# Optimization experiments

Hardware: AMD Instinct MI355X
Metric: run time of the kernel (lower is better)

## Reference

```python
import jax, jax.numpy as jnp
import numpy as np

B, N, K = 16, 2048, 20
NUM_PART = 16  # number of object classes for the one-hot label
NP = 50        # num_part (per-point part labels)
NEG_SLOPE = 0.2


def graph_feature(x, k):
    """DGCNN get_graph_feature. x: [B,C,N] -> [B,2C,N,k]."""
    xx = jnp.sum(x * x, axis=1)                      # [B,N]
    inner = jnp.einsum('bcn,bcm->bnm', x, x)         # [B,N,N]
    # negative squared distance (larger = closer)
    d = 2.0 * inner - xx[:, :, None] - xx[:, None, :]
    idx = jax.lax.top_k(d, k)[1]                     # [B,N,k] int32
    xt = jnp.transpose(x, (0, 2, 1))                 # [B,N,C]
    nbr = jax.vmap(lambda f, i: f[i])(xt, idx)       # [B,N,k,C] gather
    ctr = jnp.broadcast_to(xt[:, :, None, :], nbr.shape)
    feat = jnp.concatenate([nbr - ctr, ctr], axis=-1)  # [B,N,k,2C]
    return jnp.transpose(feat, (0, 3, 1, 2))         # [B,2C,N,k]


def cbr2d(x, w, s, b):  # 1x1 conv2d + folded-BN affine + leaky_relu
    y = jnp.einsum('oc,bcnk->bonk', w, x)
    return jax.nn.leaky_relu(y * s[None, :, None, None] + b[None, :, None, None], NEG_SLOPE)


def cbr1d(x, w, s, b):  # 1x1 conv1d + folded-BN affine + leaky_relu
    y = jnp.einsum('oc,bcn->bon', w, x)
    return jax.nn.leaky_relu(y * s[None, :, None] + b[None, :, None], NEG_SLOPE)


def setup_inputs() -> dict:
    key = jax.random.key(0)
    ks = jax.random.split(key, 40)
    ki = iter(range(40))

    def w(shape):
        fan_in = shape[1]
        return jax.random.normal(ks[next(ki)], shape, jnp.float32) * np.float32(np.sqrt(2.0 / fan_in))

    def sb(c):
        s = 1.0 + 0.1 * jax.random.normal(ks[next(ki)], (c,), jnp.float32)
        b = 0.1 * jax.random.normal(ks[next(ki)], (c,), jnp.float32)
        return s, b

    inp = {}
    inp['points'] = jax.random.normal(ks[next(ki)], (B, 3, N), jnp.float32)
    cls = jax.random.randint(ks[next(ki)], (B,), 0, NUM_PART)
    inp['cls_label'] = jax.nn.one_hot(cls, NUM_PART, dtype=jnp.float32)

    inp['w1'] = w((64, 6));    inp['s1'], inp['b1'] = sb(64)
    inp['w2'] = w((64, 64));   inp['s2'], inp['b2'] = sb(64)
    inp['w3'] = w((64, 128));  inp['s3'], inp['b3'] = sb(64)
    inp['w4'] = w((64, 64));   inp['s4'], inp['b4'] = sb(64)
    inp['w5'] = w((64, 128));  inp['s5'], inp['b5'] = sb(64)
    inp['w6'] = w((1024, 192)); inp['s6'], inp['b6'] = sb(1024)
    inp['wc'] = w((64, 16));   inp['sc'], inp['bc'] = sb(64)
    inp['wf1'] = w((256, 1024 + 64 + 192)); inp['sf1'], inp['bf1'] = sb(256)
    inp['wf2'] = w((256, 256)); inp['sf2'], inp['bf2'] = sb(256)
    inp['wf3'] = w((128, 256)); inp['sf3'], inp['bf3'] = sb(128)
    inp['wf4'] = w((NP, 128))
    return inp


def reference(points, cls_label,
              w1, s1, b1, w2, s2, b2, w3, s3, b3, w4, s4, b4, w5, s5, b5,
              w6, s6, b6, wc, sc, bc,
              wf1, sf1, bf1, wf2, sf2, bf2, wf3, sf3, bf3, wf4):
    # EdgeConv block 1
    x = graph_feature(points, K)                # [B,6,N,K]
    x = cbr2d(x, w1, s1, b1)
    x = cbr2d(x, w2, s2, b2)
    x1 = jnp.max(x, axis=-1)                    # [B,64,N]
    # EdgeConv block 2
    x = graph_feature(x1, K)                    # [B,128,N,K]
    x = cbr2d(x, w3, s3, b3)
    x = cbr2d(x, w4, s4, b4)
    x2 = jnp.max(x, axis=-1)
    # EdgeConv block 3
    x = graph_feature(x2, K)
    x = cbr2d(x, w5, s5, b5)
    x3 = jnp.max(x, axis=-1)

    xc = jnp.concatenate([x1, x2, x3], axis=1)  # [B,192,N]
    g = cbr1d(xc, w6, s6, b6)                   # [B,1024,N]
    g = jnp.max(g, axis=-1, keepdims=True)      # [B,1024,1]
    g = jnp.broadcast_to(g, (g.shape[0], 1024, N))

    oh = jnp.broadcast_to(cls_label[:, :, None], (cls_label.shape[0], 16, N))
    cv = cbr1d(oh, wc, sc, bc)                  # [B,64,N]

    x = jnp.concatenate([g, cv, x1, x2, x3], axis=1)  # [B,1280,N]
    feat = cbr1d(x, wf1, sf1, bf1)              # dropout = identity (eval)
    feat = cbr1d(feat, wf2, sf2, bf2)
    feat = cbr1d(feat, wf3, sf3, bf3)
    out = jnp.einsum('oc,bcn->bon', wf4, feat)  # [B,NP,N]
    out = jax.nn.log_softmax(out, axis=1)
    return jnp.transpose(out, (0, 2, 1))        # [B,N,NP]
```

## Files before the change

kernel.cpp:

```cpp
#include <hip/hip_runtime.h>

constexpr int PTS = 2048;
constexpr int KK  = 20;

typedef __attribute__((ext_vector_type(8))) short bf8;
typedef __attribute__((ext_vector_type(4))) float f32x4;

static __device__ __forceinline__ float lrelu(float x) { return fmaxf(x, 0.2f * x); }
static __device__ __forceinline__ float rl(float v, int l) {
  return __int_as_float(__builtin_amdgcn_readlane(__float_as_int(v), l));
}
static __device__ __forceinline__ unsigned cvt2(float lo, float hi) {
  unsigned r;
  asm("v_cvt_pk_bf16_f32 %0, %1, %2" : "=v"(r) : "v"(lo), "v"(hi));
  return r;
}
static __device__ __forceinline__ unsigned cvt2lo(float a, float b, unsigned h) {
  return cvt2(a - __uint_as_float(h << 16), b - __uint_as_float(h & 0xffff0000u));
}
static __device__ __forceinline__ unsigned short rne_bf16(float v) {
  unsigned u = __float_as_uint(v);
  return (unsigned short)((u + 0x7fffu + ((u >> 16) & 1u)) >> 16);
}
static __device__ __forceinline__ float bf2f(unsigned short u) {
  return __uint_as_float(((unsigned)u) << 16);
}
static __device__ __forceinline__ int swz(int row, int slot) {
  return slot ^ (row & 3) ^ ((row >> 2) & 3);
}
static __device__ __forceinline__ void argmax64(float& v, int& m) {
#pragma unroll
  for (int mask = 1; mask < 64; mask <<= 1) {
    float ov = __shfl_xor(v, mask, 64);
    int om = __shfl_xor(m, mask, 64);
    if (ov > v || (ov == v && om < m)) { v = ov; m = om; }
  }
}

template <int C>
__global__ __launch_bounds__(256) void xnorm_k(const float* __restrict__ x, float* __restrict__ xx) {
  const int i = blockIdx.x * 256 + threadIdx.x;
  const int b = i >> 11, m = i & 2047;
  float s = 0.f;
#pragma unroll
  for (int c = 0; c < C; ++c) {
    const float v = x[((long long)b * C + c) * PTS + m];
    s = fmaf(v, v, s);
  }
  xx[i] = s;
}

template <int C>
__global__ __launch_bounds__(256, 4) void fknn4_k(const float* __restrict__ x, const float* __restrict__ xx,
                                                  int* __restrict__ idxout) {
  __shared__ float dist[4][2112];
  __shared__ float xns[4][68];
  const int tid = threadIdx.x, lane = tid & 63, wid = tid >> 6;
  const int b = blockIdx.y;
  const int n0 = blockIdx.x * 4;

  if (tid < 4 * C) {
    const int p = tid & 3, c = tid >> 2;
    xns[p][c] = x[((long long)b * C + c) * PTS + n0 + p];
  }
  __syncthreads();

  float acc[4][2][4] = {};
  const float* px0 = x + (long long)b * C * PTS + (2 * wid) * 256 + 4 * lane;
  const float* px1 = px0 + 256;
#pragma unroll 4
  for (int c = 0; c < C; ++c) {
    const f32x4 v0 = *(const f32x4*)(px0 + (long long)c * PTS);
    const f32x4 v1 = *(const f32x4*)(px1 + (long long)c * PTS);
    const float xn0 = xns[0][c], xn1 = xns[1][c], xn2 = xns[2][c], xn3 = xns[3][c];
#pragma unroll
    for (int i = 0; i < 4; ++i) {
      acc[0][0][i] = fmaf(xn0, v0[i], acc[0][0][i]);
      acc[1][0][i] = fmaf(xn1, v0[i], acc[1][0][i]);
      acc[2][0][i] = fmaf(xn2, v0[i], acc[2][0][i]);
      acc[3][0][i] = fmaf(xn3, v0[i], acc[3][0][i]);
      acc[0][1][i] = fmaf(xn0, v1[i], acc[0][1][i]);
      acc[1][1][i] = fmaf(xn1, v1[i], acc[1][1][i]);
      acc[2][1][i] = fmaf(xn2, v1[i], acc[2][1][i]);
      acc[3][1][i] = fmaf(xn3, v1[i], acc[3][1][i]);
    }
  }
#pragma unroll
  for (int tt = 0; tt < 2; ++tt) {
    const f32x4 xv = *(const f32x4*)&xx[b * 2048 + (2 * wid + tt) * 256 + 4 * lane];
#pragma unroll
    for (int p = 0; p < 4; ++p)
#pragma unroll
      for (int i = 0; i < 4; ++i)
        dist[p][lane * 33 + 8 * wid + 4 * tt + i] = 2.f * acc[p][tt][i] - xv[i];
  }
  __syncthreads();

  const float NEG = -3.4e38f;
  float* dp = dist[wid];
  const int n = n0 + wid;
#define LDD(r) float d##r = dp[lane * 33 + r];
  LDD(0) LDD(1) LDD(2) LDD(3) LDD(4) LDD(5) LDD(6) LDD(7)
  LDD(8) LDD(9) LDD(10) LDD(11) LDD(12) LDD(13) LDD(14) LDD(15)
  LDD(16) LDD(17) LDD(18) LDD(19) LDD(20) LDD(21) LDD(22) LDD(23)
  LDD(24) LDD(25) LDD(26) LDD(27) LDD(28) LDD(29) LDD(30) LDD(31)
#undef LDD

#define P2(vA, iA, vB, iB, vO, iO) float vO = vA; int iO = iA; if (vB > vA) { vO = vB; iO = iB; }
#define TREE32(bvout, bsout)                                                            \
  {                                                                                     \
    P2(d0, 0, d1, 1, e0, j0) P2(d2, 2, d3, 3, e1, j1) P2(d4, 4, d5, 5, e2, j2)          \
    P2(d6, 6, d7, 7, e3, j3) P2(d8, 8, d9, 9, e4, j4) P2(d10, 10, d11, 11, e5, j5)      \
    P2(d12, 12, d13, 13, e6, j6) P2(d14, 14, d15, 15, e7, j7)                           \
    P2(d16, 16, d17, 17, e8, j8) P2(d18, 18, d19, 19, e9, j9)                           \
    P2(d20, 20, d21, 21, e10, j10) P2(d22, 22, d23, 23, e11, j11)                       \
    P2(d24, 24, d25, 25, e12, j12) P2(d26, 26, d27, 27, e13, j13)                       \
    P2(d28, 28, d29, 29, e14, j14) P2(d30, 30, d31, 31, e15, j15)                       \
    P2(e0, j0, e1, j1, f0, k0) P2(e2, j2, e3, j3, f1, k1)                               \
    P2(e4, j4, e5, j5, f2, k2) P2(e6, j6, e7, j7, f3, k3)                               \
    P2(e8, j8, e9, j9, f4, k4) P2(e10, j10, e11, j11, f5, k5)                           \
    P2(e12, j12, e13, j13, f6, k6) P2(e14, j14, e15, j15, f7, k7)                       \
    P2(f0, k0, f1, k1, g0, l0) P2(f2, k2, f3, k3, g1, l1)                               \
    P2(f4, k4, f5, k5, g2, l2) P2(f6, k6, f7, k7, g3, l3)                               \
    P2(g0, l0, g1, l1, h0, q0) P2(g2, l2, g3, l3, h1, q1)                               \
    P2(h0, q0, h1, q1, tf, ti)                                                          \
    bvout = tf;                                                                         \
    bsout = ti;                                                                         \
  }

  float c1v, c2v, c3v;
  int c1s, c2s, c3s;
  TREE32(c1v, c1s)
#define INVR(r) d##r = (c1s == r) ? NEG : d##r;
  INVR(0) INVR(1) INVR(2) INVR(3) INVR(4) INVR(5) INVR(6) INVR(7)
  INVR(8) INVR(9) INVR(10) INVR(11) INVR(12) INVR(13) INVR(14) INVR(15)
  INVR(16) INVR(17) INVR(18) INVR(19) INVR(20) INVR(21) INVR(22) INVR(23)
  INVR(24) INVR(25) INVR(26) INVR(27) INVR(28) INVR(29) INVR(30) INVR(31)
#undef INVR
  TREE32(c2v, c2s)
#define INVR(r) d##r = (c2s == r) ? NEG : d##r;
  INVR(0) INVR(1) INVR(2) INVR(3) INVR(4) INVR(5) INVR(6) INVR(7)
  INVR(8) INVR(9) INVR(10) INVR(11) INVR(12) INVR(13) INVR(14) INVR(15)
  INVR(16) INVR(17) INVR(18) INVR(19) INVR(20) INVR(21) INVR(22) INVR(23)
  INVR(24) INVR(25) INVR(26) INVR(27) INVR(28) INVR(29) INVR(30) INVR(31)
#undef INVR
  TREE32(c3v, c3s)
#define INVR(r) d##r = (c3s == r) ? NEG : d##r;
  INVR(0) INVR(1) INVR(2) INVR(3) INVR(4) INVR(5) INVR(6) INVR(7)
  INVR(8) INVR(9) INVR(10) INVR(11) INVR(12) INVR(13) INVR(14) INVR(15)
  INVR(16) INVR(17) INVR(18) INVR(19) INVR(20) INVR(21) INVR(22) INVR(23)
  INVR(24) INVR(25) INVR(26) INVR(27) INVR(28) INVR(29) INVR(30) INVR(31)
#undef INVR
  int c1m = ((c1s >> 2) << 8) + 4 * lane + (c1s & 3);
  int c2m = ((c2s >> 2) << 8) + 4 * lane + (c2s & 3);
  int c3m = ((c3s >> 2) << 8) + 4 * lane + (c3s & 3);

  int keep = 0;
  for (int rd = 0; rd < KK; ++rd) {
    float cv = c1v; int cm = c1m;
    argmax64(cv, cm);
    if (lane == rd) keep = cm;
    const int ol = (cm >> 2) & 63;
    const bool own = (lane == ol);
    if (own) { c1v = c2v; c1m = c2m; c2v = c3v; c2m = c3m; c3v = NEG; }
    const float oc1 = __shfl(c1v, ol, 64);
    if (oc1 == NEG) {
      float nv; int ns;
      TREE32(nv, ns)
      const int nm = ((ns >> 2) << 8) + 4 * lane + (ns & 3);
      if (own) { c1v = nv; c1m = nm; }
#define INVO(r) d##r = (own && ns == r) ? NEG : d##r;
      INVO(0) INVO(1) INVO(2) INVO(3) INVO(4) INVO(5) INVO(6) INVO(7)
      INVO(8) INVO(9) INVO(10) INVO(11) INVO(12) INVO(13) INVO(14) INVO(15)
      INVO(16) INVO(17) INVO(18) INVO(19) INVO(20) INVO(21) INVO(22) INVO(23)
      INVO(24) INVO(25) INVO(26) INVO(27) INVO(28) INVO(29) INVO(30) INVO(31)
#undef INVO
    }
  }
#undef TREE32
#undef P2
  if (lane < KK) idxout[((long long)b * PTS + n) * KK + lane] = keep;
}

__global__ __launch_bounds__(256) void prep_k(
    const float* __restrict__ w3, const float* __restrict__ s3, const float* __restrict__ b3,
    const float* __restrict__ w5, const float* __restrict__ s5, const float* __restrict__ b5,
    float* __restrict__ wc3, float* __restrict__ sc3, float* __restrict__ bc3,
    float* __restrict__ wc5, float* __restrict__ sc5, float* __restrict__ bc5) {
  const int i = blockIdx.x * 256 + threadIdx.x;
  const int half = i >> 13;
  const int r = i & 8191;
  const float* w = half ? w5 : w3;
  float* wcp = half ? wc5 : wc3;
  const int o = r >> 6, c = r & 63;
  wcp[r] = (o < 64) ? w[o * 128 + c] : (w[(o - 64) * 128 + 64 + c] - w[(o - 64) * 128 + c]);
  if (r < 128) {
    const float* s = half ? s5 : s3;
    const float* bb = half ? b5 : b3;
    float* scp = half ? sc5 : sc3;
    float* bcp = half ? bc5 : bc3;
    scp[r] = s[r & 63];
    bcp[r] = (r < 64) ? 0.f : bb[r - 64];
  }
}

__global__ __launch_bounds__(256) void wsplit_k(const float* __restrict__ w2, const float* __restrict__ w4,
                                                unsigned short* __restrict__ W2hi, unsigned short* __restrict__ W2lo,
                                                unsigned short* __restrict__ W4hi, unsigned short* __restrict__ W4lo) {
  const int i = blockIdx.x * 256 + threadIdx.x;
  const float v = (i < 4096) ? w2[i] : w4[i - 4096];
  const unsigned short h = rne_bf16(v);
  const unsigned short l = rne_bf16(v - bf2f(h));
  if (i < 4096) { W2hi[i] = h; W2lo[i] = l; }
  else { W4hi[i - 4096] = h; W4lo[i - 4096] = l; }
}

__global__ __launch_bounds__(256) void pq1_k(const float* __restrict__ pts,
    const float* __restrict__ w1, const float* __restrict__ s1, const float* __restrict__ b1,
    float* __restrict__ PQ) {
  const int i = blockIdx.x * 256 + threadIdx.x;
  const int o = i & 63;
  const int bn = i >> 6;
  const int b = bn >> 11, n = bn & 2047;
  const float* pb = pts + (long long)b * 3 * PTS;
  const float x = pb[n], y = pb[PTS + n], z = pb[2 * PTS + n];
  const float s = s1[o];
  const float wa0 = w1[o * 6], wa1 = w1[o * 6 + 1], wa2 = w1[o * 6 + 2];
  const float wb0 = w1[o * 6 + 3], wb1 = w1[o * 6 + 4], wb2 = w1[o * 6 + 5];
  PQ[(long long)bn * 128 + o] = s * (wa0 * x + wa1 * y + wa2 * z);
  PQ[(long long)bn * 128 + 64 + o] =
      fmaf(s, (wb0 - wa0) * x + (wb1 - wa1) * y + (wb2 - wa2) * z, b1[o]);
}

static __device__ __forceinline__ void mkfrag2(const float4 p0, const float4 p1,
                                               const float4 q0, const float4 q1,
                                               bf8& hi, bf8& lo) {
  const float y[8] = {p0.x + q0.x, p0.y + q0.y, p0.z + q0.z, p0.w + q0.w,
                      p1.x + q1.x, p1.y + q1.y, p1.z + q1.z, p1.w + q1.w};
  union { unsigned u[4]; bf8 v; } rh, rlo;
#pragma unroll
  for (int i = 0; i < 4; ++i) {
    const float a = lrelu(y[2 * i]), b = lrelu(y[2 * i + 1]);
    const unsigned h = cvt2(a, b);
    rh.u[i] = h;
    rlo.u[i] = cvt2lo(a, b, h);
  }
  hi = rh.v; lo = rlo.v;
}

__global__ __launch_bounds__(256) void edgemf_k(
    const float* __restrict__ PQ, const int* __restrict__ idxb,
    const unsigned short* __restrict__ Whi, const unsigned short* __restrict__ Wlo,
    const float* __restrict__ s2v, const float* __restrict__ b2v,
    float* __restrict__ outC) {
  const int lane = threadIdx.x & 63, wid = threadIdx.x >> 6;
  const int g = blockIdx.x;
  const int b = g >> 8;
  const int n0 = (g & 255) * 8 + wid * 2;
  bf8 wbh[4][2], wbl[4][2];
#pragma unroll
  for (int nf = 0; nf < 4; ++nf)
#pragma unroll
    for (int kt = 0; kt < 2; ++kt) {
      const int off = (16 * nf + (lane & 15)) * 64 + kt * 32 + (lane >> 4) * 8;
      wbh[nf][kt] = *(const bf8*)&Whi[off];
      wbl[nf][kt] = *(const bf8*)&Wlo[off];
    }
  const float* Pb = PQ + (long long)b * PTS * 128;
  const int co = (lane >> 4) * 8;
  int mm[2][2];
  float4 qa[2][2], qb[2][2];
#pragma unroll
  for (int pt = 0; pt < 2; ++pt) {
    const int n = n0 + pt;
    const int* ir = idxb + ((long long)b * PTS + n) * KK;
    const int j1 = 16 + (lane & 15);
    mm[pt][0] = ir[lane & 15];
    mm[pt][1] = ir[j1 < KK ? j1 : 0];
    qa[pt][0] = *(const float4*)&Pb[n * 128 + 64 + co];
    qb[pt][0] = *(const float4*)&Pb[n * 128 + 68 + co];
    qa[pt][1] = *(const float4*)&Pb[n * 128 + 96 + co];
    qb[pt][1] = *(const float4*)&Pb[n * 128 + 100 + co];
  }
  f32x4 acc[4][4] = {};
#pragma unroll
  for (int pt = 0; pt < 2; ++pt) {
#pragma unroll
    for (int f = 0; f < 2; ++f) {
      const int m = mm[pt][f];
      const float4 p0a = *(const float4*)&Pb[m * 128 + co];
      const float4 p0b = *(const float4*)&Pb[m * 128 + 4 + co];
      const float4 p1a = *(const float4*)&Pb[m * 128 + 32 + co];
      const float4 p1b = *(const float4*)&Pb[m * 128 + 36 + co];
      bf8 a0h, a0l, a1h, a1l;
      mkfrag2(p0a, p0b, qa[pt][0], qb[pt][0], a0h, a0l);
      mkfrag2(p1a, p1b, qa[pt][1], qb[pt][1], a1h, a1l);
      const int mf = pt * 2 + f;
#pragma unroll
      for (int nf = 0; nf < 4; ++nf) {
        acc[mf][nf] = __builtin_amdgcn_mfma_f32_16x16x32_bf16(a0h, wbh[nf][0], acc[mf][nf], 0, 0, 0);
        acc[mf][nf] = __builtin_amdgcn_mfma_f32_16x16x32_bf16(a0l, wbh[nf][0], acc[mf][nf], 0, 0, 0);
        acc[mf][nf] = __builtin_amdgcn_mfma_f32_16x16x32_bf16(a0h, wbl[nf][0], acc[mf][nf], 0, 0, 0);
      }
#pragma unroll
      for (int nf = 0; nf < 4; ++nf) {
        acc[mf][nf] = __builtin_amdgcn_mfma_f32_16x16x32_bf16(a1h, wbh[nf][1], acc[mf][nf], 0, 0, 0);
        acc[mf][nf] = __builtin_amdgcn_mfma_f32_16x16x32_bf16(a1l, wbh[nf][1], acc[mf][nf], 0, 0, 0);
        acc[mf][nf] = __builtin_amdgcn_mfma_f32_16x16x32_bf16(a1h, wbl[nf][1], acc[mf][nf], 0, 0, 0);
      }
    }
  }
#pragma unroll
  for (int nf = 0; nf < 4; ++nf) {
    const int o = 16 * nf + (lane & 15);
    const float so = s2v[o], bo = b2v[o];
#pragma unroll
    for (int pt = 0; pt < 2; ++pt) {
      float v = -3.4e38f;
#pragma unroll
      for (int f = 0; f < 2; ++f) {
        const int mf = pt * 2 + f;
#pragma unroll
        for (int r = 0; r < 4; ++r) v = fmaxf(v, lrelu(fmaf(so, acc[mf][nf][r], bo)));
      }
      v = fmaxf(v, __shfl_xor(v, 16, 64));
      v = fmaxf(v, __shfl_xor(v, 32, 64));
      if ((lane >> 4) == 0) outC[((long long)b * 64 + o) * PTS + n0 + pt] = v;
    }
  }
}

__global__ __launch_bounds__(256) void edge3f_k(const float* __restrict__ PQ,
                                                const int* __restrict__ idxb, float* __restrict__ outC) {
  const int lane = threadIdx.x & 63, wid = threadIdx.x >> 6;
  const int g = blockIdx.x;
  const int b = g >> 6, n0 = ((g & 63) << 5) + (wid << 3);
  const float* Pb = PQ + (long long)b * PTS * 128;
  for (int pt = 0; pt < 8; ++pt) {
    const int n = n0 + pt;
    const float qv = Pb[n * 128 + 64 + lane];
    const int* ir = idxb + ((long long)b * PTS + n) * KK;
    float gm = -3.4e38f;
#pragma unroll 4
    for (int j = 0; j < KK; ++j) {
      const int m = ir[j];
      gm = fmaxf(gm, lrelu(Pb[m * 128 + lane] + qv));
    }
    outC[((long long)b * 64 + lane) * PTS + n] = gm;
  }
}

struct SrcTab { const float* p[4]; long long bs[4]; };

template <int MODE, int SPLIT>
__global__ __launch_bounds__(256) void mfgemm_k(
    const float* __restrict__ W, int wstride, int c0, SrcTab tab, int C,
    const float* __restrict__ sv, const float* __restrict__ bv, const float* __restrict__ tadd,
    float* __restrict__ out, int O) {
  __shared__ __align__(16) short Wl[(1 + SPLIT) * 128 * 32];
  __shared__ __align__(16) short Xl[(1 + SPLIT) * 128 * 32];
  __shared__ float red[2][128];
  const int tid = threadIdx.x, lane = tid & 63, wid = tid >> 6;
  const int nt = blockIdx.x, ot = blockIdx.y, b = blockIdx.z;
  const int n0 = nt * 128, o0 = ot * 128;
  const int wm = wid >> 1, wn = wid & 1;
  f32x4 acc[4][4] = {};
  for (int cc = 0; cc < C; cc += 32) {
    __syncthreads();
    {
      const int o = tid >> 1, hf = tid & 1;
      const float* src = &W[(long long)(o0 + o) * wstride + c0 + cc + hf * 16];
      const float4 v0 = *(const float4*)src;
      const float4 v1 = *(const float4*)(src + 4);
      const float4 v2 = *(const float4*)(src + 8);
      const float4 v3 = *(const float4*)(src + 12);
      uint4 d0, d1;
      d0.x = cvt2(v0.x, v0.y); d0.y = cvt2(v0.z, v0.w);
      d0.z = cvt2(v1.x, v1.y); d0.w = cvt2(v1.z, v1.w);
      d1.x = cvt2(v2.x, v2.y); d1.y = cvt2(v2.z, v2.w);
      d1.z = cvt2(v3.x, v3.y); d1.w = cvt2(v3.z, v3.w);
      *(uint4*)&Wl[o * 32 + swz(o, hf * 2) * 8] = d0;
      *(uint4*)&Wl[o * 32 + swz(o, hf * 2 + 1) * 8] = d1;
      if (SPLIT) {
        uint4 e0, e1;
        e0.x = cvt2lo(v0.x, v0.y, d0.x); e0.y = cvt2lo(v0.z, v0.w, d0.y);
        e0.z = cvt2lo(v1.x, v1.y, d0.z); e0.w = cvt2lo(v1.z, v1.w, d0.w);
        e1.x = cvt2lo(v2.x, v2.y, d1.x); e1.y = cvt2lo(v2.z, v2.w, d1.y);
        e1.z = cvt2lo(v3.x, v3.y, d1.z); e1.w = cvt2lo(v3.z, v3.w, d1.w);
        *(uint4*)&Wl[4096 + o * 32 + swz(o, hf * 2) * 8] = e0;
        *(uint4*)&Wl[4096 + o * 32 + swz(o, hf * 2 + 1) * 8] = e1;
      }
    }
    {
      const int n = tid & 127, ch = (tid >> 7) * 16;
      float val[16];
#pragma unroll
      for (int i = 0; i < 16; ++i) {
        const int cg = cc + ch + i;
        val[i] = tab.p[cg >> 6][tab.bs[cg >> 6] * b + (long long)(cg & 63) * PTS + n0 + n];
      }
      uint4 d0, d1;
      d0.x = cvt2(val[0], val[1]);   d0.y = cvt2(val[2], val[3]);
      d0.z = cvt2(val[4], val[5]);   d0.w = cvt2(val[6], val[7]);
      d1.x = cvt2(val[8], val[9]);   d1.y = cvt2(val[10], val[11]);
      d1.z = cvt2(val[12], val[13]); d1.w = cvt2(val[14], val[15]);
      const int s0 = ch >> 3;
      *(uint4*)&Xl[n * 32 + swz(n, s0) * 8] = d0;
      *(uint4*)&Xl[n * 32 + swz(n, s0 + 1) * 8] = d1;
      if (SPLIT) {
        uint4 e0, e1;
        e0.x = cvt2lo(val[0], val[1], d0.x);   e0.y = cvt2lo(val[2], val[3], d0.y);
        e0.z = cvt2lo(val[4], val[5], d0.z);   e0.w = cvt2lo(val[6], val[7], d0.w);
        e1.x = cvt2lo(val[8], val[9], d1.x);   e1.y = cvt2lo(val[10], val[11], d1.y);
        e1.z = cvt2lo(val[12], val[13], d1.z); e1.w = cvt2lo(val[14], val[15], d1.w);
        *(uint4*)&Xl[4096 + n * 32 + swz(n, s0) * 8] = e0;
        *(uint4*)&Xl[4096 + n * 32 + swz(n, s0 + 1) * 8] = e1;
      }
    }
    __syncthreads();
    bf8 afh[4], bfh[4], afl[4], bfl[4];
#pragma unroll
    for (int mf = 0; mf < 4; ++mf) {
      const int arow = wm * 64 + mf * 16 + (lane & 15);
      const int aoff = arow * 32 + swz(arow, lane >> 4) * 8;
      afh[mf] = *(const bf8*)&Wl[aoff];
      if (SPLIT) afl[mf] = *(const bf8*)&Wl[4096 + aoff];
    }
#pragma unroll
    for (int nf = 0; nf < 4; ++nf) {
      const int brow = wn * 64 + nf * 16 + (lane & 15);
      const int boff = brow * 32 + swz(brow, lane >> 4) * 8;
      bfh[nf] = *(const bf8*)&Xl[boff];
      if (SPLIT) bfl[nf] = *(const bf8*)&Xl[4096 + boff];
    }
#pragma unroll
    for (int mf = 0; mf < 4; ++mf)
#pragma unroll
      for (int nf = 0; nf < 4; ++nf) {
        acc[mf][nf] = __builtin_amdgcn_mfma_f32_16x16x32_bf16(afh[mf], bfh[nf], acc[mf][nf], 0, 0, 0);
        if (SPLIT) {
          acc[mf][nf] = __builtin_amdgcn_mfma_f32_16x16x32_bf16(afl[mf], bfh[nf], acc[mf][nf], 0, 0, 0);
          acc[mf][nf] = __builtin_amdgcn_mfma_f32_16x16x32_bf16(afh[mf], bfl[nf], acc[mf][nf], 0, 0, 0);
        }
      }
  }
  if (MODE == 1) {
#pragma unroll
    for (int mf = 0; mf < 4; ++mf)
#pragma unroll
      for (int r = 0; r < 4; ++r) {
        const int orl = wm * 64 + mf * 16 + (lane >> 4) * 4 + r;
        const int o = o0 + orl;
        const float s = sv[o], bb = bv[o];
        float v = -3.4e38f;
#pragma unroll
        for (int nf = 0; nf < 4; ++nf) v = fmaxf(v, lrelu(fmaf(s, acc[mf][nf][r], bb)));
        v = fmaxf(v, __shfl_xor(v, 1, 64));
        v = fmaxf(v, __shfl_xor(v, 2, 64));
        v = fmaxf(v, __shfl_xor(v, 4, 64));
        v = fmaxf(v, __shfl_xor(v, 8, 64));
        if ((lane & 15) == 0) red[wn][orl] = v;
      }
    __syncthreads();
    if (tid < 128) {
      const float m = fmaxf(red[0][tid], red[1][tid]);
      out[((long long)b * 16 + nt) * 1024 + o0 + tid] = m;
    }
  } else if (MODE == 0) {
#pragma unroll
    for (int mf = 0; mf < 4; ++mf)
#pragma unroll
      for (int r = 0; r < 4; ++r) {
        const int o = o0 + wm * 64 + mf * 16 + (lane >> 4) * 4 + r;
        const float s = sv[o], bb = bv[o];
        const float tv = (tadd != nullptr) ? tadd[(long long)b * O + o] : 0.f;
        float* op = out + ((long long)b * O + o) * PTS + n0 + wn * 64 + (lane & 15);
#pragma unroll
        for (int nf = 0; nf < 4; ++nf)
          op[nf * 16] = lrelu(fmaf(s, acc[mf][nf][r] + tv, bb));
      }
  } else if (MODE == 2) {
#pragma unroll
    for (int mf = 0; mf < 4; ++mf) {
      const int ob = wm * 64 + mf * 16 + (lane >> 4) * 4;
      float s4[4], b4[4];
#pragma unroll
      for (int r = 0; r < 4; ++r) { s4[r] = sv[o0 + ob + r]; b4[r] = bv[o0 + ob + r]; }
#pragma unroll
      for (int nf = 0; nf < 4; ++nf) {
        const int n = n0 + wn * 64 + nf * 16 + (lane & 15);
        float4 v;
        v.x = lrelu(fmaf(s4[0], acc[mf][nf][0], b4[0]));
        v.y = lrelu(fmaf(s4[1], acc[mf][nf][1], b4[1]));
        v.z = lrelu(fmaf(s4[2], acc[mf][nf][2], b4[2]));
        v.w = lrelu(fmaf(s4[3], acc[mf][nf][3], b4[3]));
        *(float4*)&out[((long long)b * PTS + n) * O + o0 + ob] = v;
      }
    }
  } else {
#pragma unroll
    for (int mf = 0; mf < 4; ++mf) {
      const int ob = wm * 64 + mf * 16 + (lane >> 4) * 4;
      float s4[4], b4[4];
#pragma unroll
      for (int r = 0; r < 4; ++r) { s4[r] = sv[o0 + ob + r]; b4[r] = bv[o0 + ob + r]; }
#pragma unroll
      for (int nf = 0; nf < 4; ++nf) {
        const int n = n0 + wn * 64 + nf * 16 + (lane & 15);
        float4 v;
        v.x = fmaf(s4[0], acc[mf][nf][0], b4[0]);
        v.y = fmaf(s4[1], acc[mf][nf][1], b4[1]);
        v.z = fmaf(s4[2], acc[mf][nf][2], b4[2]);
        v.w = fmaf(s4[3], acc[mf][nf][3], b4[3]);
        *(float4*)&out[((long long)b * PTS + n) * O + o0 + ob] = v;
      }
    }
  }
}

__global__ __launch_bounds__(256) void tvec_k(
    const float* __restrict__ cls, const float* __restrict__ wc, const float* __restrict__ sc,
    const float* __restrict__ bc, const float* __restrict__ gp, const float* __restrict__ wf1,
    float* __restrict__ tvec) {
  __shared__ float gs[1024];
  __shared__ float cvs[64];
  const int b = blockIdx.x, tid = threadIdx.x;
  for (int q = tid; q < 1024; q += 256) {
    float m = -3.4e38f;
#pragma unroll 4
    for (int t = 0; t < 16; ++t) m = fmaxf(m, gp[((long long)b * 16 + t) * 1024 + q]);
    gs[q] = m;
  }
  if (tid < 64) {
    float a = 0.f;
#pragma unroll
    for (int j = 0; j < 16; ++j) a = fmaf(wc[tid * 16 + j], cls[b * 16 + j], a);
    cvs[tid] = lrelu(fmaf(sc[tid], a, bc[tid]));
  }
  __syncthreads();
  const float* wr = wf1 + (long long)tid * 1280;
  float a0 = 0.f, a1 = 0.f;
  for (int c = 0; c < 1024; c += 4) {
    const float4 w = *(const float4*)&wr[c];
    const float4 gv = *(const float4*)&gs[c];
    a0 = fmaf(w.x, gv.x, a0); a1 = fmaf(w.y, gv.y, a1);
    a0 = fmaf(w.z, gv.z, a0); a1 = fmaf(w.w, gv.w, a1);
  }
#pragma unroll
  for (int c = 0; c < 64; c += 4) {
    const float4 w = *(const float4*)&wr[1024 + c];
    const float4 cv = *(const float4*)&cvs[c];
    a0 = fmaf(w.x, cv.x, a0); a1 = fmaf(w.y, cv.y, a1);
    a0 = fmaf(w.z, cv.z, a0); a1 = fmaf(w.w, cv.w, a1);
  }
  tvec[b * 256 + tid] = a0 + a1;
}

__global__ __launch_bounds__(256) void logits_k(const float* __restrict__ f3t, const float* __restrict__ wf4,
                                                float* __restrict__ out) {
  __shared__ float wT[6464];
  const int tid = threadIdx.x, lane = tid & 63, wv = tid >> 6;
  for (int q = tid; q < 6400; q += 256) {
    const int o = q >> 7, c = q & 127;
    wT[c * 50 + o] = wf4[q];
  }
  __syncthreads();
  const long long pn = (long long)blockIdx.x * 4 + wv;
  const float lo = f3t[pn * 128 + lane], hi = f3t[pn * 128 + 64 + lane];
  float a0 = 0.f, a1 = 0.f;
#pragma unroll
  for (int c = 0; c < 64; c += 2) {
    a0 = fmaf(wT[c * 50 + lane], rl(lo, c), a0);
    a1 = fmaf(wT[(c + 1) * 50 + lane], rl(lo, c + 1), a1);
  }
#pragma unroll
  for (int c = 0; c < 64; c += 2) {
    a0 = fmaf(wT[(64 + c) * 50 + lane], rl(hi, c), a0);
    a1 = fmaf(wT[(65 + c) * 50 + lane], rl(hi, c + 1), a1);
  }
  const float logit = (lane < 50) ? (a0 + a1) : -3.4e38f;
  float M = logit;
#pragma unroll
  for (int mask = 1; mask < 64; mask <<= 1) M = fmaxf(M, __shfl_xor(M, mask, 64));
  const float ex = (lane < 50) ? __expf(logit - M) : 0.f;
  float S = ex;
#pragma unroll
  for (int mask = 1; mask < 64; mask <<= 1) S += __shfl_xor(S, mask, 64);
  if (lane < 50) out[pn * 50 + lane] = logit - M - __logf(S);
}

extern "C" void kernel_launch(void* const* d_in, const int* in_sizes, int n_in,
                              void* d_out, int out_size, void* d_ws, size_t ws_size,
                              hipStream_t stream) {
  (void)in_sizes; (void)n_in; (void)out_size; (void)ws_size;
  const float* points = (const float*)d_in[0];
  const float* cls = (const float*)d_in[1];
  const float* w1 = (const float*)d_in[2];
  const float* s1 = (const float*)d_in[3];
  const float* b1 = (const float*)d_in[4];
  const float* w2 = (const float*)d_in[5];
  const float* s2 = (const float*)d_in[6];
  const float* b2 = (const float*)d_in[7];
  const float* w3 = (const float*)d_in[8];
  const float* s3 = (const float*)d_in[9];
  const float* b3 = (const float*)d_in[10];
  const float* w4 = (const float*)d_in[11];
  const float* s4 = (const float*)d_in[12];
  const float* b4 = (const float*)d_in[13];
  const float* w5 = (const float*)d_in[14];
  const float* s5 = (const float*)d_in[15];
  const float* b5 = (const float*)d_in[16];
  const float* w6 = (const float*)d_in[17];
  const float* s6 = (const float*)d_in[18];
  const float* b6 = (const float*)d_in[19];
  const float* wc = (const float*)d_in[20];
  const float* sc = (const float*)d_in[21];
  const float* bc = (const float*)d_in[22];
  const float* wf1 = (const float*)d_in[23];
  const float* sf1 = (const float*)d_in[24];
  const float* bf1 = (const float*)d_in[25];
  const float* wf2 = (const float*)d_in[26];
  const float* sf2 = (const float*)d_in[27];
  const float* bf2 = (const float*)d_in[28];
  const float* wf3 = (const float*)d_in[29];
  const float* sf3 = (const float*)d_in[30];
  const float* bf3 = (const float*)d_in[31];
  const float* wf4 = (const float*)d_in[32];
  float* out = (float*)d_out;
  float* ws = (float*)d_ws;

  float* x1c = ws;
  float* x2c = ws + 2097152LL;
  float* x3c = ws + 4194304LL;
  float* f1c = ws + 8388608LL;
  float* f2c = ws;
  float* f3t = ws + 8388608LL;
  float* PQf = ws + 8388608LL;
  int* idx = (int*)(ws + 16777216LL);
  float* xxb = ws + 17432576LL;
  float* gpart = ws + 17465344LL;
  float* tvec = ws + 17743872LL;
  float* wc3 = ws + 17747968LL;
  float* sc3 = ws + 17756160LL;
  float* bc3 = ws + 17756288LL;
  float* wc5 = ws + 17756416LL;
  float* sc5 = ws + 17764608LL;
  float* bc5 = ws + 17764736LL;
  unsigned short* W2hi = (unsigned short*)(ws + 17764864LL);
  unsigned short* W2lo = (unsigned short*)(ws + 17766912LL);
  unsigned short* W4hi = (unsigned short*)(ws + 17768960LL);
  unsigned short* W4lo = (unsigned short*)(ws + 17771008LL);

  SrcTab tabX{{x1c, x2c, x3c, nullptr}, {64LL * PTS, 64LL * PTS, 64LL * PTS, 0}};
  SrcTab tabX1{{x1c, nullptr, nullptr, nullptr}, {64LL * PTS, 0, 0, 0}};
  SrcTab tabX2{{x2c, nullptr, nullptr, nullptr}, {64LL * PTS, 0, 0, 0}};
  SrcTab tabF1{{f1c, f1c + 64 * PTS, f1c + 128 * PTS, f1c + 192 * PTS},
               {256LL * PTS, 256LL * PTS, 256LL * PTS, 256LL * PTS}};
  SrcTab tabF2{{f2c, f2c + 64 * PTS, f2c + 128 * PTS, f2c + 192 * PTS},
               {256LL * PTS, 256LL * PTS, 256LL * PTS, 256LL * PTS}};

  prep_k<<<64, 256, 0, stream>>>(w3, s3, b3, w5, s5, b5, wc3, sc3, bc3, wc5, sc5, bc5);
  wsplit_k<<<32, 256, 0, stream>>>(w2, w4, W2hi, W2lo, W4hi, W4lo);

  xnorm_k<3><<<128, 256, 0, stream>>>(points, xxb);
  fknn4_k<3><<<dim3(512, 16), 256, 0, stream>>>(points, xxb, idx);
  pq1_k<<<8192, 256, 0, stream>>>(points, w1, s1, b1, PQf);
  edgemf_k<<<4096, 256, 0, stream>>>(PQf, idx, W2hi, W2lo, s2, b2, x1c);

  xnorm_k<64><<<128, 256, 0, stream>>>(x1c, xxb);
  fknn4_k<64><<<dim3(512, 16), 256, 0, stream>>>(x1c, xxb, idx);
  mfgemm_k<3, 1><<<dim3(16, 1, 16), 256, 0, stream>>>(wc3, 64, 0, tabX1, 64, sc3, bc3, nullptr, PQf, 128);
  edgemf_k<<<4096, 256, 0, stream>>>(PQf, idx, W4hi, W4lo, s4, b4, x2c);

  xnorm_k<64><<<128, 256, 0, stream>>>(x2c, xxb);
  fknn4_k<64><<<dim3(512, 16), 256, 0, stream>>>(x2c, xxb, idx);
  mfgemm_k<3, 1><<<dim3(16, 1, 16), 256, 0, stream>>>(wc5, 64, 0, tabX2, 64, sc5, bc5, nullptr, PQf, 128);
  edge3f_k<<<1024, 256, 0, stream>>>(PQf, idx, x3c);

  mfgemm_k<1, 1><<<dim3(16, 8, 16), 256, 0, stream>>>(w6, 192, 0, tabX, 192, s6, b6, nullptr, gpart, 1024);
  tvec_k<<<16, 256, 0, stream>>>(cls, wc, sc, bc, gpart, wf1, tvec);
  mfgemm_k<0, 1><<<dim3(16, 2, 16), 256, 0, stream>>>(wf1, 1280, 1088, tabX, 192, sf1, bf1, tvec, f1c, 256);
  mfgemm_k<0, 1><<<dim3(16, 2, 16), 256, 0, stream>>>(wf2, 256, 0, tabF1, 256, sf2, bf2, nullptr, f2c, 256);
  mfgemm_k<2, 1><<<dim3(16, 1, 16), 256, 0, stream>>>(wf3, 256, 0, tabF2, 256, sf3, bf3, nullptr, f3t, 128);
  logits_k<<<8192, 256, 0, stream>>>(f3t, wf4, out);
}
```

Baseline: 1.061 ms.

## Compute 64-channel kNN distances with split-bf16 MFMA on transposed features

Adds an xsplit kernel that transposes the 64-channel features into point-major layout, split into bf16 high and low parts. It also adds fknn5_k, which computes the inner products with 16x16x32 bf16 MFMA instructions using three cross terms (hi·hi, lo·hi, hi·lo) to stay close to fp32 accuracy. The top-20 selection is moved into a shared select20 helper. The aim is to replace the scalar FMA dot-product loop of the EdgeConv 2 and 3 kNN with matrix-core work. In exchange it adds an extra split kernel and scratch traffic, wastes 12 of the 16 MFMA rows, and carries a small risk of near-tie neighbor reordering from reduced precision.

```diff
diff --git a/kernel.cpp b/kernel.cpp
--- a/kernel.cpp
+++ b/kernel.cpp
@@ -37,75 +37,14 @@
   }
 }
 
-template <int C>
-__global__ __launch_bounds__(256) void xnorm_k(const float* __restrict__ x, float* __restrict__ xx) {
-  const int i = blockIdx.x * 256 + threadIdx.x;
-  const int b = i >> 11, m = i & 2047;
-  float s = 0.f;
-#pragma unroll
-  for (int c = 0; c < C; ++c) {
-    const float v = x[((long long)b * C + c) * PTS + m];
-    s = fmaf(v, v, s);
-  }
-  xx[i] = s;
-}
-
-template <int C>
-__global__ __launch_bounds__(256, 4) void fknn4_k(const float* __restrict__ x, const float* __restrict__ xx,
-                                                  int* __restrict__ idxout) {
-  __shared__ float dist[4][2112];
-  __shared__ float xns[4][68];
-  const int tid = threadIdx.x, lane = tid & 63, wid = tid >> 6;
-  const int b = blockIdx.y;
-  const int n0 = blockIdx.x * 4;
-
-  if (tid < 4 * C) {
-    const int p = tid & 3, c = tid >> 2;
-    xns[p][c] = x[((long long)b * C + c) * PTS + n0 + p];
-  }
-  __syncthreads();
-
-  float acc[4][2][4] = {};
-  const float* px0 = x + (long long)b * C * PTS + (2 * wid) * 256 + 4 * lane;
-  const float* px1 = px0 + 256;
-#pragma unroll 4
-  for (int c = 0; c < C; ++c) {
-    const f32x4 v0 = *(const f32x4*)(px0 + (long long)c * PTS);
-    const f32x4 v1 = *(const f32x4*)(px1 + (long long)c * PTS);
-    const float xn0 = xns[0][c], xn1 = xns[1][c], xn2 = xns[2][c], xn3 = xns[3][c];
-#pragma unroll
-    for (int i = 0; i < 4; ++i) {
-      acc[0][0][i] = fmaf(xn0, v0[i], acc[0][0][i]);
-      acc[1][0][i] = fmaf(xn1, v0[i], acc[1][0][i]);
-      acc[2][0][i] = fmaf(xn2, v0[i], acc[2][0][i]);
-      acc[3][0][i] = fmaf(xn3, v0[i], acc[3][0][i]);
-      acc[0][1][i] = fmaf(xn0, v1[i], acc[0][1][i]);
-      acc[1][1][i] = fmaf(xn1, v1[i], acc[1][1][i]);
-      acc[2][1][i] = fmaf(xn2, v1[i], acc[2][1][i]);
-      acc[3][1][i] = fmaf(xn3, v1[i], acc[3][1][i]);
-    }
-  }
-#pragma unroll
-  for (int tt = 0; tt < 2; ++tt) {
-    const f32x4 xv = *(const f32x4*)&xx[b * 2048 + (2 * wid + tt) * 256 + 4 * lane];
-#pragma unroll
-    for (int p = 0; p < 4; ++p)
-#pragma unroll
-      for (int i = 0; i < 4; ++i)
-        dist[p][lane * 33 + 8 * wid + 4 * tt + i] = 2.f * acc[p][tt][i] - xv[i];
-  }
-  __syncthreads();
-
+static __device__ __forceinline__ int select20(float* __restrict__ dp, const int lane) {
   const float NEG = -3.4e38f;
-  float* dp = dist[wid];
-  const int n = n0 + wid;
 #define LDD(r) float d##r = dp[lane * 33 + r];
   LDD(0) LDD(1) LDD(2) LDD(3) LDD(4) LDD(5) LDD(6) LDD(7)
   LDD(8) LDD(9) LDD(10) LDD(11) LDD(12) LDD(13) LDD(14) LDD(15)
   LDD(16) LDD(17) LDD(18) LDD(19) LDD(20) LDD(21) LDD(22) LDD(23)
   LDD(24) LDD(25) LDD(26) LDD(27) LDD(28) LDD(29) LDD(30) LDD(31)
 #undef LDD
-
 #define P2(vA, iA, vB, iB, vO, iO) float vO = vA; int iO = iA; if (vB > vA) { vO = vB; iO = iB; }
 #define TREE32(bvout, bsout)                                                            \
   {                                                                                     \
@@ -127,7 +66,6 @@
     bvout = tf;                                                                         \
     bsout = ti;                                                                         \
   }
-
   float c1v, c2v, c3v;
   int c1s, c2s, c3s;
   TREE32(c1v, c1s)
@@ -179,7 +117,141 @@
   }
 #undef TREE32
 #undef P2
-  if (lane < KK) idxout[((long long)b * PTS + n) * KK + lane] = keep;
+  return keep;
+}
+
+template <int C>
+__global__ __launch_bounds__(256) void xnorm_k(const float* __restrict__ x, float* __restrict__ xx) {
+  const int i = blockIdx.x * 256 + threadIdx.x;
+  const int b = i >> 11, m = i & 2047;
+  float s = 0.f;
+#pragma unroll
+  for (int c = 0; c < C; ++c) {
+    const float v = x[((long long)b * C + c) * PTS + m];
+    s = fmaf(v, v, s);
+  }
+  xx[i] = s;
+}
+
+__global__ __launch_bounds__(256) void xsplit_k(const float* __restrict__ xc,
+                                                unsigned short* __restrict__ Th,
+                                                unsigned short* __restrict__ Tl) {
+  const int i = blockIdx.x * 256 + threadIdx.x;
+  const int b = i >> 11, m = i & 2047;
+  const float* src = xc + (long long)b * 64 * PTS + m;
+  ushort4* th = (ushort4*)(Th + (long long)i * 64);
+  ushort4* tl = (ushort4*)(Tl + (long long)i * 64);
+#pragma unroll
+  for (int c4 = 0; c4 < 16; ++c4) {
+    const float v0 = src[(long long)(4 * c4 + 0) * PTS];
+    const float v1 = src[(long long)(4 * c4 + 1) * PTS];
+    const float v2 = src[(long long)(4 * c4 + 2) * PTS];
+    const float v3 = src[(long long)(4 * c4 + 3) * PTS];
+    ushort4 h, l;
+    h.x = rne_bf16(v0); l.x = rne_bf16(v0 - bf2f(h.x));
+    h.y = rne_bf16(v1); l.y = rne_bf16(v1 - bf2f(h.y));
+    h.z = rne_bf16(v2); l.z = rne_bf16(v2 - bf2f(h.z));
+    h.w = rne_bf16(v3); l.w = rne_bf16(v3 - bf2f(h.w));
+    th[c4] = h;
+    tl[c4] = l;
+  }
+}
+
+template <int C>
+__global__ __launch_bounds__(256, 4) void fknn4_k(const float* __restrict__ x, const float* __restrict__ xx,
+                                                  int* __restrict__ idxout) {
+  __shared__ float dist[4][2112];
+  __shared__ float xns[4][68];
+  const int tid = threadIdx.x, lane = tid & 63, wid = tid >> 6;
+  const int b = blockIdx.y;
+  const int n0 = blockIdx.x * 4;
+
+  if (tid < 4 * C) {
+    const int p = tid & 3, c = tid >> 2;
+    xns[p][c] = x[((long long)b * C + c) * PTS + n0 + p];
+  }
+  __syncthreads();
+
+  float acc[4][2][4] = {};
+  const float* px0 = x + (long long)b * C * PTS + (2 * wid) * 256 + 4 * lane;
+  const float* px1 = px0 + 256;
+#pragma unroll 4
+  for (int c = 0; c < C; ++c) {
+    const f32x4 v0 = *(const f32x4*)(px0 + (long long)c * PTS);
+    const f32x4 v1 = *(const f32x4*)(px1 + (long long)c * PTS);
+    const float xn0 = xns[0][c], xn1 = xns[1][c], xn2 = xns[2][c], xn3 = xns[3][c];
+#pragma unroll
+    for (int i = 0; i < 4; ++i) {
+      acc[0][0][i] = fmaf(xn0, v0[i], acc[0][0][i]);
+      acc[1][0][i] = fmaf(xn1, v0[i], acc[1][0][i]);
+      acc[2][0][i] = fmaf(xn2, v0[i], acc[2][0][i]);
+      acc[3][0][i] = fmaf(xn3, v0[i], acc[3][0][i]);
+      acc[0][1][i] = fmaf(xn0, v1[i], acc[0][1][i]);
+      acc[1][1][i] = fmaf(xn1, v1[i], acc[1][1][i]);
+      acc[2][1][i] = fmaf(xn2, v1[i], acc[2][1][i]);
+      acc[3][1][i] = fmaf(xn3, v1[i], acc[3][1][i]);
+    }
+  }
+#pragma unroll
+  for (int tt = 0; tt < 2; ++tt) {
+    const f32x4 xv = *(const f32x4*)&xx[b * 2048 + (2 * wid + tt) * 256 + 4 * lane];
+#pragma unroll
+    for (int p = 0; p < 4; ++p)
+#pragma unroll
+      for (int i = 0; i < 4; ++i)
+        dist[p][lane * 33 + 8 * wid + 4 * tt + i] = 2.f * acc[p][tt][i] - xv[i];
+  }
+  __syncthreads();
+
+  const int keep = select20(dist[wid], lane);
+  if (lane < KK) idxout[((long long)b * PTS + n0 + wid) * KK + lane] = keep;
+}
+
+__global__ __launch_bounds__(256, 4) void fknn5_k(const unsigned short* __restrict__ Thg,
+                                                  const unsigned short* __restrict__ Tlg,
+                                                  const float* __restrict__ xx,
+                                                  int* __restrict__ idxout) {
+  __shared__ float dist[4][2112];
+  const int tid = threadIdx.x, lane = tid & 63, wid = tid >> 6;
+  const int b = blockIdx.y;
+  const int n0 = blockIdx.x * 4;
+  const unsigned short* Th = Thg + (long long)b * PTS * 64;
+  const unsigned short* Tl = Tlg + (long long)b * PTS * 64;
+  const int ko = (lane >> 4) * 8;
+  const int arow0 = n0 + (lane & 15);
+  const int ar = (arow0 < PTS) ? arow0 : (PTS - 1);
+  bf8 Ah0 = *(const bf8*)&Th[ar * 64 + ko];
+  bf8 Ah1 = *(const bf8*)&Th[ar * 64 + 32 + ko];
+  bf8 Al0 = *(const bf8*)&Tl[ar * 64 + ko];
+  bf8 Al1 = *(const bf8*)&Tl[ar * 64 + 32 + ko];
+  const int mw = wid * 512;
+  for (int mt = 0; mt < 32; ++mt) {
+    const int mbase = mw + mt * 16;
+    const int brow = mbase + (lane & 15);
+    const bf8 Bh0 = *(const bf8*)&Th[brow * 64 + ko];
+    const bf8 Bh1 = *(const bf8*)&Th[brow * 64 + 32 + ko];
+    const bf8 Bl0 = *(const bf8*)&Tl[brow * 64 + ko];
+    const bf8 Bl1 = *(const bf8*)&Tl[brow * 64 + 32 + ko];
+    f32x4 acc = {0.f, 0.f, 0.f, 0.f};
+    acc = __builtin_amdgcn_mfma_f32_16x16x32_bf16(Ah0, Bh0, acc, 0, 0, 0);
+    acc = __builtin_amdgcn_mfma_f32_16x16x32_bf16(Al0, Bh0, acc, 0, 0, 0);
+    acc = __builtin_amdgcn_mfma_f32_16x16x32_bf16(Ah0, Bl0, acc, 0, 0, 0);
+    acc = __builtin_amdgcn_mfma_f32_16x16x32_bf16(Ah1, Bh1, acc, 0, 0, 0);
+    acc = __builtin_amdgcn_mfma_f32_16x16x32_bf16(Al1, Bh1, acc, 0, 0, 0);
+    acc = __builtin_amdgcn_mfma_f32_16x16x32_bf16(Ah1, Bl1, acc, 0, 0, 0);
+    if (lane < 16) {
+      const int m = mbase + lane;
+      const float xv = xx[b * 2048 + m];
+      const int addr = ((m >> 2) & 63) * 33 + ((m >> 8) << 2) + (m & 3);
+#pragma unroll
+      for (int r = 0; r < 4; ++r)
+        dist[r][addr] = 2.f * acc[r] - xv;
+    }
+  }
+  __syncthreads();
+
+  const int keep = select20(dist[wid], lane);
+  if (lane < KK) idxout[((long long)b * PTS + n0 + wid) * KK + lane] = keep;
 }
 
 __global__ __launch_bounds__(256) void prep_k(
@@ -636,6 +708,8 @@
   float* f2c = ws;
   float* f3t = ws + 8388608LL;
   float* PQf = ws + 8388608LL;
+  unsigned short* xThi = (unsigned short*)(ws + 8388608LL);
+  unsigned short* xTlo = (unsigned short*)(ws + 9437184LL);
   int* idx = (int*)(ws + 16777216LL);
   float* xxb = ws + 17432576LL;
   float* gpart = ws + 17465344LL;
@@ -668,12 +742,14 @@
   edgemf_k<<<4096, 256, 0, stream>>>(PQf, idx, W2hi, W2lo, s2, b2, x1c);
 
   xnorm_k<64><<<128, 256, 0, stream>>>(x1c, xxb);
-  fknn4_k<64><<<dim3(512, 16), 256, 0, stream>>>(x1c, xxb, idx);
+  xsplit_k<<<128, 256, 0, stream>>>(x1c, xThi, xTlo);
+  fknn5_k<<<dim3(512, 16), 256, 0, stream>>>(xThi, xTlo, xxb, idx);
   mfgemm_k<3, 1><<<dim3(16, 1, 16), 256, 0, stream>>>(wc3, 64, 0, tabX1, 64, sc3, bc3, nullptr, PQf, 128);
   edgemf_k<<<4096, 256, 0, stream>>>(PQf, idx, W4hi, W4lo, s4, b4, x2c);
 
   xnorm_k<64><<<128, 256, 0, stream>>>(x2c, xxb);
-  fknn4_k<64><<<dim3(512, 16), 256, 0, stream>>>(x2c, xxb, idx);
+  xsplit_k<<<128, 256, 0, stream>>>(x2c, xThi, xTlo);
+  fknn5_k<<<dim3(512, 16), 256, 0, stream>>>(xThi, xTlo, xxb, idx);
   mfgemm_k<3, 1><<<dim3(16, 1, 16), 256, 0, stream>>>(wc5, 64, 0, tabX2, 64, sc5, bc5, nullptr, PQf, 128);
   edge3f_k<<<1024, 256, 0, stream>>>(PQf, idx, x3c);
 
```

Measured after the change: 1.738 ms. 63.8% more time.
